# Optimization experiments

Measured on AMD Instinct MI355X. Metric: run time of the kernel, lower is better.

Reference implementation:

```python
import jax, jax.numpy as jnp
import numpy as np

R = 16
ALPHA = 32
SCALING = ALPHA / R  # 2.0


def setup_inputs() -> dict:
    key = jax.random.key(0)
    k_x, k_w, k_b, k_a, k_bm = jax.random.split(key, 5)
    d = 1024
    x = jax.random.normal(k_x, (4, 4096, d), dtype=jnp.float32)
    W = jax.random.normal(k_w, (d, d), dtype=jnp.float32) * 0.02
    b = jax.random.normal(k_b, (d,), dtype=jnp.float32) * 0.02
    A = jax.random.normal(k_a, (R, d), dtype=jnp.float32) * 0.02
    B = jax.random.normal(k_bm, (d, R), dtype=jnp.float32) * 0.02
    return {"x": x, "W": W, "b": b, "A": A, "B": B}


def reference(x, W, b, A, B):
    # base linear: x @ W^T + b   (W: [out, in])
    base = jnp.einsum("bsd,od->bso", x, W) + b
    # low-rank update: (x @ A^T) @ B^T, scaled (dropout p=0 -> identity)
    u = jnp.einsum("bsd,rd->bsr", x, A)   # [B, S, r]
    update = jnp.einsum("bsr,or->bso", u, B)
    return base + SCALING * update
```

## Files before the change

kernel.cpp:

```cpp
#include <hip/hip_runtime.h>


typedef __bf16 bf16x8 __attribute__((ext_vector_type(8)));
typedef float f32x4 __attribute__((ext_vector_type(4)));
typedef unsigned short ushort8 __attribute__((ext_vector_type(8)));

__device__ __forceinline__ unsigned short f2bf(float f) {
    __bf16 h = (__bf16)f;
    union { __bf16 b; unsigned short u; } v; v.b = h; return v.u;
}
__device__ __forceinline__ ushort8 cvt8(f32x4 a, f32x4 b) {
    ushort8 o;
#pragma unroll
    for (int i = 0; i < 4; ++i) { o[i] = f2bf(a[i]); o[i + 4] = f2bf(b[i]); }
    return o;
}
__device__ __forceinline__ void gld16(const unsigned short* g, unsigned short* l) {
    __builtin_amdgcn_global_load_lds(
        (const __attribute__((address_space(1))) unsigned int*)g,
        (__attribute__((address_space(3))) unsigned int*)l, 16, 0, 0);
}

__global__ __launch_bounds__(256) void prep(
    const float* __restrict__ X, const float* __restrict__ W,
    const float* __restrict__ A, const float* __restrict__ B,
    unsigned short* __restrict__ xbf, unsigned short* __restrict__ Weff)
{
    const int b = blockIdx.x;
    if (b < 512) {
        const int idx = b * 256 + threadIdx.x;
        const int o  = idx >> 7;
        const int kc = (idx & 127) << 3;
        float br[16];
#pragma unroll
        for (int r = 0; r < 16; ++r) br[r] = 2.0f * B[o * 16 + r];
        float acc[8];
        const float* wrow = W + (size_t)o * 1024 + kc;
#pragma unroll
        for (int j = 0; j < 8; ++j) acc[j] = wrow[j];
#pragma unroll
        for (int r = 0; r < 16; ++r) {
            const float* arow = A + r * 1024 + kc;
#pragma unroll
            for (int j = 0; j < 8; ++j) acc[j] += br[r] * arow[j];
        }
        ushort8 o8;
#pragma unroll
        for (int j = 0; j < 8; ++j) o8[j] = f2bf(acc[j]);
        *(ushort8*)(Weff + (size_t)o * 1024 + kc) = o8;
    } else {
        const size_t i = ((size_t)(b - 512) * 256 + threadIdx.x) * 8;
        f32x4 a = *(const f32x4*)(X + i);
        f32x4 c = *(const f32x4*)(X + i + 4);
        *(ushort8*)(xbf + i) = cvt8(a, c);
    }
}

template <bool XF32>
__global__ __launch_bounds__(256) void gemm_bt(
    const void* __restrict__ X_,
    const unsigned short* __restrict__ Wt,
    const float* __restrict__ bias,
    float* __restrict__ out)
{
    __shared__ __align__(16) unsigned short lA[128 * 32];
    __shared__ __align__(16) unsigned short lB[128 * 32];

    const int t    = threadIdx.x;
    const int lane = t & 63;
    const int w    = t >> 6;
    const int bm   = blockIdx.x * 128;
    const int bn   = blockIdx.y * 128;
    const int wm   = (w & 1) * 64;
    const int wn   = (w >> 1) * 64;
    const int r16  = lane & 15;
    const int quad = lane >> 4;

    const int srow = t >> 2;
    const int gc   = (t & 3) ^ ((srow >> 1) & 3);
    unsigned short* lsA = lA + t * 8;
    unsigned short* lsB = lB + t * 8;
    const size_t ga0 = (size_t)(bm + srow) * 1024 + gc * 8;
    const size_t ga1 = (size_t)(bm + srow + 64) * 1024 + gc * 8;
    const unsigned short* gB0 = Wt + (size_t)(bn + srow) * 1024 + gc * 8;

    const int p    = (quad ^ ((r16 >> 1) & 3)) * 8;
    const int aoff = (wm + r16) * 32 + p;
    const int boff = (wn + r16) * 32 + p;

    const unsigned short* Xb = (const unsigned short*)X_;
    const float*          Xf = (const float*)X_;

    f32x4 acc[4][4];
#pragma unroll
    for (int i = 0; i < 4; ++i)
#pragma unroll
        for (int j = 0; j < 4; ++j) {
            f32x4 z = {0.f, 0.f, 0.f, 0.f};
            acc[i][j] = z;
        }

    for (int kt = 0; kt < 1024; kt += 32) {
        if (XF32) {
            f32x4 a0 = *(const f32x4*)(Xf + ga0 + kt);
            f32x4 a1 = *(const f32x4*)(Xf + ga0 + kt + 4);
            f32x4 a2 = *(const f32x4*)(Xf + ga1 + kt);
            f32x4 a3 = *(const f32x4*)(Xf + ga1 + kt + 4);
            *(ushort8*)lsA          = cvt8(a0, a1);
            *(ushort8*)(lsA + 2048) = cvt8(a2, a3);
        } else {
            gld16(Xb + ga0 + kt, lsA);
            gld16(Xb + ga1 + kt, lsA + 2048);
        }
        gld16(gB0 + kt,             lsB);
        gld16(gB0 + kt + 64 * 1024, lsB + 2048);
        __syncthreads();

        bf16x8 fa[4], fb[4];
#pragma unroll
        for (int mt = 0; mt < 4; ++mt) fa[mt] = *(const bf16x8*)(lA + aoff + mt * 16 * 32);
#pragma unroll
        for (int nt = 0; nt < 4; ++nt) fb[nt] = *(const bf16x8*)(lB + boff + nt * 16 * 32);

#pragma unroll
        for (int mt = 0; mt < 4; ++mt)
#pragma unroll
            for (int nt = 0; nt < 4; ++nt)
                acc[mt][nt] = __builtin_amdgcn_mfma_f32_16x16x32_bf16(
                    fa[mt], fb[nt], acc[mt][nt], 0, 0, 0);

        __syncthreads();
    }

    const int orow0 = bm + wm + quad * 4;
    const int ocol0 = bn + wn + r16;
#pragma unroll
    for (int nt = 0; nt < 4; ++nt) {
        const float bv = bias[ocol0 + nt * 16];
#pragma unroll
        for (int mt = 0; mt < 4; ++mt)
#pragma unroll
            for (int i = 0; i < 4; ++i)
                out[(size_t)(orow0 + mt * 16 + i) * 1024 + (ocol0 + nt * 16)] =
                    acc[mt][nt][i] + bv;
    }
}

extern "C" void kernel_launch(void* const* d_in, const int* in_sizes, int n_in,
                              void* d_out, int out_size, void* d_ws, size_t ws_size,
                              hipStream_t stream) {
    const float* x  = (const float*)d_in[0];
    const float* W  = (const float*)d_in[1];
    const float* b  = (const float*)d_in[2];
    const float* A  = (const float*)d_in[3];
    const float* Bm = (const float*)d_in[4];
    float* out = (float*)d_out;

    const int M = in_sizes[0] / 1024;
    dim3 grid(M / 128, 1024 / 128);

    const bool fast = ws_size >= ((size_t)(M)*1024*2 + (2u << 20) + 4096);
    if (fast) {
        unsigned short* xbf  = (unsigned short*)d_ws;
        unsigned short* Weff = xbf + (size_t)M * 1024;
        hipLaunchKernelGGL(prep, dim3(512 + M / 2), dim3(256), 0, stream,
                           x, W, A, Bm, xbf, Weff);
        hipLaunchKernelGGL((gemm_bt<false>), grid, dim3(256), 0, stream,
                           (const void*)xbf, Weff, b, out);
    } else {
        unsigned short* Weff = (unsigned short*)d_ws;
        hipLaunchKernelGGL(prep, dim3(512), dim3(256), 0, stream,
                           x, W, A, Bm, (unsigned short*)nullptr, Weff);
        hipLaunchKernelGGL((gemm_bt<true>), grid, dim3(256), 0, stream,
                           (const void*)x, Weff, b, out);
    }
}
```

Before: 166.6 us.

## Replace 128x128 GEMM with 256x256 double-buffered 8-wave pipelined kernel

Adds a new bf16 GEMM kernel with 256x256 output tiles, 512 threads and a 64-wide K step. It double-buffers 128KB of LDS and issues global-to-LDS prefetches two K steps ahead, interleaved with four MFMA phases that are bracketed by barriers and setprio. Block indices are swizzled for L2 locality, and the fast path now requires M to be a multiple of 256. The goal is more data reuse per tile and overlap of memory traffic with MFMA work. In exchange it uses heavy LDS, relies on manual vmcnt accounting, and leaves only 256 blocks, which may underfill the CUs.

```diff
diff --git a/kernel.cpp b/kernel.cpp
--- a/kernel.cpp
+++ b/kernel.cpp
@@ -20,6 +20,9 @@
         (const __attribute__((address_space(1))) unsigned int*)g,
         (__attribute__((address_space(3))) unsigned int*)l, 16, 0, 0);
 }
+
+#define FENCE() asm volatile("" ::: "memory")
+#define BARRIER() do { FENCE(); __builtin_amdgcn_s_barrier(); FENCE(); } while (0)
 
 __global__ __launch_bounds__(256) void prep(
     const float* __restrict__ X, const float* __restrict__ W,
@@ -56,12 +59,159 @@
     }
 }
 
-template <bool XF32>
-__global__ __launch_bounds__(256) void gemm_bt(
-    const void* __restrict__ X_,
+template<int MH, int NH>
+__device__ __forceinline__ void qmfma(f32x4 (&acc)[8][4],
+                                      const bf16x8 (&fa)[8][2],
+                                      const bf16x8 (&fb)[4][2]) {
+#pragma unroll
+    for (int m2 = 0; m2 < 4; ++m2)
+#pragma unroll
+        for (int n2 = 0; n2 < 2; ++n2)
+#pragma unroll
+            for (int ks = 0; ks < 2; ++ks)
+                acc[MH * 4 + m2][NH * 2 + n2] = __builtin_amdgcn_mfma_f32_16x16x32_bf16(
+                    fa[MH * 4 + m2][ks], fb[NH * 2 + n2][ks],
+                    acc[MH * 4 + m2][NH * 2 + n2], 0, 0, 0);
+}
+
+#define PHASE_MFMA(MH, NH)                                          \
+    do { BARRIER();                                                 \
+         asm volatile("s_waitcnt lgkmcnt(0)" ::: "memory");         \
+         __builtin_amdgcn_sched_barrier(0);            \
+         __builtin_amdgcn_s_setprio(1);                             \
+         qmfma<MH, NH>(acc, fa, fb);                                \
+         __builtin_amdgcn_s_setprio(0);                             \
+         BARRIER(); } while (0)
+
+__global__ __launch_bounds__(512, 2) void gemm256(
+    const unsigned short* __restrict__ Xb,
     const unsigned short* __restrict__ Wt,
     const float* __restrict__ bias,
     float* __restrict__ out)
+{
+    extern __shared__ __align__(16) unsigned short lds[];
+
+    const int t    = threadIdx.x;
+    const int lane = t & 63;
+    const int w    = t >> 6;
+    const int wr   = w >> 2;
+    const int wc   = w & 3;
+    const int r16  = lane & 15;
+    const int quad = lane >> 4;
+
+    const int nwg = gridDim.x;
+    int swz = blockIdx.x;
+    if ((nwg & 7) == 0) swz = (swz & 7) * (nwg >> 3) + (swz >> 3);
+    const int bm = (swz >> 2) * 256;
+    const int bn = (swz & 3) * 256;
+
+    const int c0 = w * 128 + lane, c1 = c0 + 64;
+    const int r0 = c0 >> 3,        r1 = c1 >> 3;
+    const int s0c = (c0 & 7) ^ (r0 & 7);
+    const int s1c = (c1 & 7) ^ (r1 & 7);
+    const unsigned short* pA0 = Xb + (size_t)(bm + r0) * 1024 + s0c * 8;
+    const unsigned short* pA1 = Xb + (size_t)(bm + r1) * 1024 + s1c * 8;
+    const unsigned short* pB0 = Wt + (size_t)(bn + r0) * 1024 + s0c * 8;
+    const unsigned short* pB1 = Wt + (size_t)(bn + r1) * 1024 + s1c * 8;
+    const int lc0 = c0 * 8, lc1 = c1 * 8;
+
+    const int ck    = (quad ^ (r16 & 7)) * 8;
+    const int aBase = wr * 8192 + r16 * 64 + ck;
+    const int bBase = 16384 + (wc >> 1) * 8192 + (wc & 1) * 4096 + r16 * 64 + ck;
+
+    f32x4 acc[8][4];
+#pragma unroll
+    for (int i = 0; i < 8; ++i)
+#pragma unroll
+        for (int jj = 0; jj < 4; ++jj)
+            acc[i][jj] = (f32x4){0.f, 0.f, 0.f, 0.f};
+
+    gld16(pA0,               lds + lc0);            gld16(pA1,               lds + lc1);            FENCE();
+    gld16(pA0 + 131072,      lds + 8192  + lc0);    gld16(pA1 + 131072,      lds + 8192  + lc1);    FENCE();
+    gld16(pB0,               lds + 16384 + lc0);    gld16(pB1,               lds + 16384 + lc1);    FENCE();
+    gld16(pB0 + 131072,      lds + 24576 + lc0);    gld16(pB1 + 131072,      lds + 24576 + lc1);    FENCE();
+    gld16(pA0 + 64,          lds + 32768 + lc0);    gld16(pA1 + 64,          lds + 32768 + lc1);    FENCE();
+    gld16(pA0 + 131072 + 64, lds + 40960 + lc0);    gld16(pA1 + 131072 + 64, lds + 40960 + lc1);    FENCE();
+    gld16(pB0 + 64,          lds + 49152 + lc0);    gld16(pB1 + 64,          lds + 49152 + lc1);
+    asm volatile("s_waitcnt vmcnt(6)" ::: "memory");
+    BARRIER();
+
+#pragma unroll 2
+    for (int j = 0; j < 16; ++j) {
+        const unsigned short* Lb = lds + (j & 1) * 32768;
+        unsigned short* Sc = lds + (j & 1) * 32768;
+        unsigned short* Sn = lds + ((j & 1) ^ 1) * 32768;
+        const int k1 = (j + 1) * 64, k2 = (j + 2) * 64;
+
+        bf16x8 fa[8][2], fb[4][2];
+
+#pragma unroll
+        for (int mt = 0; mt < 4; ++mt) {
+            fa[mt][0] = *(const bf16x8*)(Lb + aBase + mt * 1024);
+            fa[mt][1] = *(const bf16x8*)(Lb + (aBase ^ 32) + mt * 1024);
+        }
+#pragma unroll
+        for (int nt = 0; nt < 2; ++nt) {
+            fb[nt][0] = *(const bf16x8*)(Lb + bBase + nt * 1024);
+            fb[nt][1] = *(const bf16x8*)(Lb + (bBase ^ 32) + nt * 1024);
+        }
+        if (wr == 0) {
+#pragma unroll
+            for (int mt = 4; mt < 8; ++mt) {
+                fa[mt][0] = *(const bf16x8*)(Lb + aBase + mt * 1024);
+                fa[mt][1] = *(const bf16x8*)(Lb + (aBase ^ 32) + mt * 1024);
+            }
+        }
+        if (j < 15) { gld16(pB0 + 131072 + k1, Sn + 24576 + lc0);
+                      gld16(pB1 + 131072 + k1, Sn + 24576 + lc1); }
+        PHASE_MFMA(0, 0);
+
+        if (wr == 1) {
+#pragma unroll
+            for (int mt = 4; mt < 8; ++mt) {
+                fa[mt][0] = *(const bf16x8*)(Lb + aBase + mt * 1024);
+                fa[mt][1] = *(const bf16x8*)(Lb + (aBase ^ 32) + mt * 1024);
+            }
+        }
+#pragma unroll
+        for (int nt = 2; nt < 4; ++nt) {
+            fb[nt][0] = *(const bf16x8*)(Lb + bBase + nt * 1024);
+            fb[nt][1] = *(const bf16x8*)(Lb + (bBase ^ 32) + nt * 1024);
+        }
+        if (j < 14) { gld16(pA0 + k2, Sc + lc0);
+                      gld16(pA1 + k2, Sc + lc1); }
+        PHASE_MFMA(0, 1);
+
+        if (j < 14) { gld16(pA0 + 131072 + k2, Sc + 8192 + lc0);
+                      gld16(pA1 + 131072 + k2, Sc + 8192 + lc1); }
+        PHASE_MFMA(1, 1);
+
+        if (j < 14) { gld16(pB0 + k2, Sc + 16384 + lc0);
+                      gld16(pB1 + k2, Sc + 16384 + lc1); }
+        if (j < 14)       asm volatile("s_waitcnt vmcnt(6)" ::: "memory");
+        else if (j == 14) asm volatile("s_waitcnt vmcnt(0)" ::: "memory");
+        PHASE_MFMA(1, 0);
+    }
+
+    const int orow0 = bm + wr * 128 + quad * 4;
+    const int ocol0 = bn + wc * 64 + r16;
+#pragma unroll
+    for (int nt = 0; nt < 4; ++nt) {
+        const float bv = bias[ocol0 + nt * 16];
+#pragma unroll
+        for (int mt = 0; mt < 8; ++mt) {
+            float* orow = out + (size_t)(orow0 + mt * 16) * 1024 + (ocol0 + nt * 16);
+#pragma unroll
+            for (int i = 0; i < 4; ++i)
+                orow[(size_t)i * 1024] = acc[mt][nt][i] + bv;
+        }
+    }
+}
+
+template <bool XF32>
+__global__ __launch_bounds__(256) void gemm_bt(
+    const void* __restrict__ X_, const unsigned short* __restrict__ Wt,
+    const float* __restrict__ bias, float* __restrict__ out)
 {
     __shared__ __align__(16) unsigned short lA[128 * 32];
     __shared__ __align__(16) unsigned short lB[128 * 32];
@@ -157,21 +307,21 @@
     float* out = (float*)d_out;
 
     const int M = in_sizes[0] / 1024;
-    dim3 grid(M / 128, 1024 / 128);
-
-    const bool fast = ws_size >= ((size_t)(M)*1024*2 + (2u << 20) + 4096);
+
+    const bool fast = (ws_size >= ((size_t)(M)*1024*2 + (2u << 20) + 4096)) &&
+                      (M % 256 == 0);
     if (fast) {
         unsigned short* xbf  = (unsigned short*)d_ws;
         unsigned short* Weff = xbf + (size_t)M * 1024;
         hipLaunchKernelGGL(prep, dim3(512 + M / 2), dim3(256), 0, stream,
                            x, W, A, Bm, xbf, Weff);
-        hipLaunchKernelGGL((gemm_bt<false>), grid, dim3(256), 0, stream,
-                           (const void*)xbf, Weff, b, out);
+        hipLaunchKernelGGL(gemm256, dim3((M / 256) * 4), dim3(512), 131072, stream,
+                           xbf, Weff, b, out);
     } else {
         unsigned short* Weff = (unsigned short*)d_ws;
         hipLaunchKernelGGL(prep, dim3(512), dim3(256), 0, stream,
                            x, W, A, Bm, (unsigned short*)nullptr, Weff);
-        hipLaunchKernelGGL((gemm_bt<true>), grid, dim3(256), 0, stream,
+        hipLaunchKernelGGL((gemm_bt<true>), dim3(M / 128, 8), dim3(256), 0, stream,
                            (const void*)x, Weff, b, out);
     }
 }
```

Result: slower. 174.9 us (+5.0%).

## Add double-buffered 256x128 GEMM kernel with split-phase MFMA scheduling

Applied to the files above, without the earlier changes.

Replaces the bf16 GEMM on the fast path with a new 512-thread kernel using 256x128 tiles, double-buffered LDS filled by global_load_lds prefetch two k-steps ahead, and explicit barriers with waitcnt so loads overlap MFMA phases. It also raises MFMA priority with s_setprio and remaps block indices in groups of eight for cache locality. The aim is to hide global load latency that the old single-buffered kernel exposed at each k-step. The fast path now also requires M divisible by 256, and the hand-placed waitcnt and barrier ordering is fragile.

```diff
diff --git a/kernel.cpp b/kernel.cpp
--- a/kernel.cpp
+++ b/kernel.cpp
@@ -20,6 +20,9 @@
         (const __attribute__((address_space(1))) unsigned int*)g,
         (__attribute__((address_space(3))) unsigned int*)l, 16, 0, 0);
 }
+
+#define FENCE() asm volatile("" ::: "memory")
+#define BARRIER() do { FENCE(); __builtin_amdgcn_s_barrier(); FENCE(); } while (0)
 
 __global__ __launch_bounds__(256) void prep(
     const float* __restrict__ X, const float* __restrict__ W,
@@ -56,12 +59,115 @@
     }
 }
 
-template <bool XF32>
-__global__ __launch_bounds__(256) void gemm_bt(
-    const void* __restrict__ X_,
+#define PHASE_MFMA(LO)                                              \
+    do { BARRIER();                                                 \
+         asm volatile("s_waitcnt lgkmcnt(0)" ::: "memory");         \
+         __builtin_amdgcn_sched_barrier(0);            \
+         __builtin_amdgcn_s_setprio(1);                             \
+         _Pragma("unroll")                                          \
+         for (int m2 = 0; m2 < 4; ++m2)                             \
+             _Pragma("unroll")                                      \
+             for (int n2 = 0; n2 < 2; ++n2)                         \
+                 acc[(LO) + m2][n2] = __builtin_amdgcn_mfma_f32_16x16x32_bf16( \
+                     fa[(LO) + m2], fb[n2], acc[(LO) + m2][n2], 0, 0, 0);      \
+         __builtin_amdgcn_s_setprio(0);                             \
+         BARRIER(); } while (0)
+
+__global__ __launch_bounds__(512, 4) void gemm256(
+    const unsigned short* __restrict__ Xb,
     const unsigned short* __restrict__ Wt,
     const float* __restrict__ bias,
     float* __restrict__ out)
+{
+    extern __shared__ __align__(16) unsigned short lds[];
+
+    const int t    = threadIdx.x;
+    const int lane = t & 63;
+    const int w    = t >> 6;
+    const int wr   = w >> 2;
+    const int wc   = w & 3;
+    const int r16  = lane & 15;
+    const int quad = lane >> 4;
+
+    const int nwg = gridDim.x;
+    int swz = blockIdx.x;
+    if ((nwg & 7) == 0) swz = (swz & 7) * (nwg >> 3) + (swz >> 3);
+    const int bm = (swz >> 3) * 256;
+    const int bn = (swz & 7) * 128;
+
+    const int r  = t >> 2;
+    const int sc = (t & 3) ^ (r & 3);
+    const unsigned short* pA0 = Xb + (size_t)(bm + r) * 1024 + sc * 8;
+    const unsigned short* pA1 = pA0 + 131072;
+    const unsigned short* pB  = Wt + (size_t)(bn + r) * 1024 + sc * 8;
+    const int lc = t * 8;
+
+    const int sw = (quad ^ (r16 & 3)) * 8;
+    const int aB = wr * 512 + r16 * 32 + sw;
+    const int bB = wc * 512 + r16 * 32 + sw;
+
+    f32x4 acc[8][2];
+#pragma unroll
+    for (int i = 0; i < 8; ++i)
+#pragma unroll
+        for (int jj = 0; jj < 2; ++jj)
+            acc[i][jj] = (f32x4){0.f, 0.f, 0.f, 0.f};
+
+    gld16(pA0,      lds + lc);                 FENCE();
+    gld16(pB,       lds + 8192 + lc);          FENCE();
+    gld16(pA1,      lds + 4096 + lc);          FENCE();
+    gld16(pA0 + 32, lds + 12288 + lc);         FENCE();
+    gld16(pB  + 32, lds + 12288 + 8192 + lc);
+    asm volatile("s_waitcnt vmcnt(2)" ::: "memory");
+    BARRIER();
+
+#pragma unroll 2
+    for (int j = 0; j < 32; ++j) {
+        const int cur  = (j & 1) * 12288;
+        const int next = cur ^ 12288;
+        const unsigned short* Lb = lds + cur;
+        const int k1 = (j + 1) * 32, k2 = (j + 2) * 32;
+
+        bf16x8 fa[8], fb[2];
+
+#pragma unroll
+        for (int mt = 0; mt < 4; ++mt)
+            fa[mt] = *(const bf16x8*)(Lb + mt * 1024 + aB);
+#pragma unroll
+        for (int nt = 0; nt < 2; ++nt)
+            fb[nt] = *(const bf16x8*)(Lb + 8192 + nt * 2048 + bB);
+        if (j < 31) gld16(pA1 + k1, lds + next + 4096 + lc);
+        PHASE_MFMA(0);
+
+#pragma unroll
+        for (int mt = 4; mt < 8; ++mt)
+            fa[mt] = *(const bf16x8*)(Lb + 4096 + (mt - 4) * 1024 + aB);
+        if (j < 30) { gld16(pA0 + k2, lds + cur + lc);              FENCE();
+                      gld16(pB  + k2, lds + cur + 8192 + lc); }
+        if (j < 30)       asm volatile("s_waitcnt vmcnt(2)" ::: "memory");
+        else if (j == 30) asm volatile("s_waitcnt vmcnt(0)" ::: "memory");
+        PHASE_MFMA(4);
+    }
+
+    const int orow0 = bm + wr * 16 + quad * 4;
+    const int ocol0 = bn + wc * 16 + r16;
+#pragma unroll
+    for (int nt = 0; nt < 2; ++nt) {
+        const float bv = bias[ocol0 + nt * 64];
+#pragma unroll
+        for (int mt = 0; mt < 8; ++mt) {
+            float* orow = out + (size_t)(orow0 + mt * 32) * 1024 + (ocol0 + nt * 64);
+#pragma unroll
+            for (int i = 0; i < 4; ++i)
+                orow[(size_t)i * 1024] = acc[mt][nt][i] + bv;
+        }
+    }
+}
+
+template <bool XF32>
+__global__ __launch_bounds__(256) void gemm_bt(
+    const void* __restrict__ X_, const unsigned short* __restrict__ Wt,
+    const float* __restrict__ bias, float* __restrict__ out)
 {
     __shared__ __align__(16) unsigned short lA[128 * 32];
     __shared__ __align__(16) unsigned short lB[128 * 32];
@@ -157,21 +263,21 @@
     float* out = (float*)d_out;
 
     const int M = in_sizes[0] / 1024;
-    dim3 grid(M / 128, 1024 / 128);
-
-    const bool fast = ws_size >= ((size_t)(M)*1024*2 + (2u << 20) + 4096);
+
+    const bool fast = (ws_size >= ((size_t)(M)*1024*2 + (2u << 20) + 4096)) &&
+                      (M % 256 == 0);
     if (fast) {
         unsigned short* xbf  = (unsigned short*)d_ws;
         unsigned short* Weff = xbf + (size_t)M * 1024;
         hipLaunchKernelGGL(prep, dim3(512 + M / 2), dim3(256), 0, stream,
                            x, W, A, Bm, xbf, Weff);
-        hipLaunchKernelGGL((gemm_bt<false>), grid, dim3(256), 0, stream,
-                           (const void*)xbf, Weff, b, out);
+        hipLaunchKernelGGL(gemm256, dim3((M / 256) * 8), dim3(512), 49152, stream,
+                           xbf, Weff, b, out);
     } else {
         unsigned short* Weff = (unsigned short*)d_ws;
         hipLaunchKernelGGL(prep, dim3(512), dim3(256), 0, stream,
                            x, W, A, Bm, (unsigned short*)nullptr, Weff);
-        hipLaunchKernelGGL((gemm_bt<true>), grid, dim3(256), 0, stream,
+        hipLaunchKernelGGL((gemm_bt<true>), dim3(M / 128, 8), dim3(256), 0, stream,
                            (const void*)x, Weff, b, out);
     }
 }
```

New measurement: 155.6 us. 1.07x faster.

## Add triple-buffered 512-thread GEMM with async LDS loads and tile swizzle

Applied to the files above, without the earlier changes.

Replaces the single-buffered 256-thread bf16 GEMM with a 512-thread kernel that uses three LDS stages filled by global_load_lds, so the next tiles load while MFMAs run. It uses explicit vmcnt waits, raw s_barrier and setprio, and remaps block indices so blocks sharing a weight column tile run close together for L2 reuse. Each wave now computes a 32x64 output tile, which cuts register pressure to allow more resident waves. The cost is 48KB of dynamic LDS and hand-tuned wait counts that could be fragile.

```diff
diff --git a/kernel.cpp b/kernel.cpp
--- a/kernel.cpp
+++ b/kernel.cpp
@@ -9,17 +9,20 @@
     __bf16 h = (__bf16)f;
     union { __bf16 b; unsigned short u; } v; v.b = h; return v.u;
 }
-__device__ __forceinline__ ushort8 cvt8(f32x4 a, f32x4 b) {
+__device__ __forceinline__ ushort8 cvt8u(f32x4 a, f32x4 b) {
     ushort8 o;
 #pragma unroll
     for (int i = 0; i < 4; ++i) { o[i] = f2bf(a[i]); o[i + 4] = f2bf(b[i]); }
     return o;
 }
-__device__ __forceinline__ void gld16(const unsigned short* g, unsigned short* l) {
+__device__ __forceinline__ void gld16(const void* g, void* l) {
     __builtin_amdgcn_global_load_lds(
         (const __attribute__((address_space(1))) unsigned int*)g,
         (__attribute__((address_space(3))) unsigned int*)l, 16, 0, 0);
 }
+
+#define FENCE() asm volatile("" ::: "memory")
+#define BARRIER() do { FENCE(); __builtin_amdgcn_s_barrier(); FENCE(); } while (0)
 
 __global__ __launch_bounds__(256) void prep(
     const float* __restrict__ X, const float* __restrict__ W,
@@ -52,16 +55,113 @@
         const size_t i = ((size_t)(b - 512) * 256 + threadIdx.x) * 8;
         f32x4 a = *(const f32x4*)(X + i);
         f32x4 c = *(const f32x4*)(X + i + 4);
-        *(ushort8*)(xbf + i) = cvt8(a, c);
-    }
-}
-
-template <bool XF32>
-__global__ __launch_bounds__(256) void gemm_bt(
-    const void* __restrict__ X_,
+        *(ushort8*)(xbf + i) = cvt8u(a, c);
+    }
+}
+
+__global__ __launch_bounds__(512, 6) void gemm256(
+    const unsigned short* __restrict__ Xb,
     const unsigned short* __restrict__ Wt,
     const float* __restrict__ bias,
     float* __restrict__ out)
+{
+    extern __shared__ __align__(16) char lds[];
+
+    const int t    = threadIdx.x;
+    const int lane = t & 63;
+    const int w    = t >> 6;
+    const int wr   = w & 3;
+    const int wc   = w >> 2;
+    const int r16  = lane & 15;
+    const int quad = lane >> 4;
+
+    const int nwg = gridDim.x;
+    int swz = blockIdx.x;
+    if ((nwg & 7) == 0) swz = (swz & 7) * (nwg >> 3) + (swz >> 3);
+    const int bm = (swz >> 3) * 128;
+    const int bn = (swz & 7) * 128;
+
+    const int ar = t >> 2;
+    const int ac = (t & 3) ^ ((ar >> 1) & 3);
+    const unsigned short* gA = Xb + (size_t)(bm + ar) * 1024 + ac * 8;
+    const unsigned short* gB = Wt + (size_t)(bn + ar) * 1024 + ac * 8;
+    const int adst = t * 16;
+
+    const int sw = (quad ^ ((r16 >> 1) & 3)) * 16;
+    const int aB = wr * 1024 + r16 * 64 + sw;
+    const int bB = 8192 + wc * 1024 + r16 * 64 + sw;
+
+    f32x4 acc[2][4];
+#pragma unroll
+    for (int i = 0; i < 2; ++i)
+#pragma unroll
+        for (int jj = 0; jj < 4; ++jj)
+            acc[i][jj] = (f32x4){0.f, 0.f, 0.f, 0.f};
+
+#define STAGE(BUF, K)                                                           \
+    do { gld16(gA + (K), lds + (BUF) + adst);        FENCE();                   \
+         gld16(gB + (K), lds + (BUF) + 8192 + adst); FENCE(); } while (0)
+
+#define TILE(J, RB, SB, STG, VM)                                                \
+    do {                                                                        \
+        const char* Lb = lds + (RB);                                            \
+        bf16x8 fa[2], fb[4];                                                    \
+        fa[0] = *(const bf16x8*)(Lb + aB);                                      \
+        fa[1] = *(const bf16x8*)(Lb + aB + 4096);                               \
+        _Pragma("unroll")                                                       \
+        for (int nt = 0; nt < 4; ++nt)                                          \
+            fb[nt] = *(const bf16x8*)(Lb + bB + nt * 2048);                     \
+        if (STG) STAGE((SB), ((J) + 2) * 32);                                   \
+        if ((VM) == 2)      asm volatile("s_waitcnt vmcnt(2)" ::: "memory");    \
+        else if ((VM) == 0) asm volatile("s_waitcnt vmcnt(0)" ::: "memory");    \
+        asm volatile("s_waitcnt lgkmcnt(0)" ::: "memory");                      \
+        BARRIER();                                                              \
+        __builtin_amdgcn_sched_barrier(0);                         \
+        __builtin_amdgcn_s_setprio(1);                                          \
+        _Pragma("unroll")                                                       \
+        for (int mt = 0; mt < 2; ++mt)                                          \
+            _Pragma("unroll")                                                   \
+            for (int nt = 0; nt < 4; ++nt)                                      \
+                acc[mt][nt] = __builtin_amdgcn_mfma_f32_16x16x32_bf16(          \
+                    fa[mt], fb[nt], acc[mt][nt], 0, 0, 0);                      \
+        __builtin_amdgcn_s_setprio(0);                                          \
+    } while (0)
+
+    STAGE(0, 0);
+    STAGE(16384, 32);
+    asm volatile("s_waitcnt vmcnt(2)" ::: "memory");
+    BARRIER();
+
+    for (int jj = 0; jj < 30; jj += 3) {
+        TILE(jj + 0, 0,     32768, 1, 2);
+        TILE(jj + 1, 16384, 0,     1, 2);
+        TILE(jj + 2, 32768, 16384, 1, 2);
+    }
+    TILE(30, 0,     0, 0, 0);
+    TILE(31, 16384, 0, 0, -1);
+
+#undef TILE
+#undef STAGE
+
+    const int orow0 = bm + wr * 16 + quad * 4;
+    const int ocol0 = bn + wc * 16 + r16;
+#pragma unroll
+    for (int nt = 0; nt < 4; ++nt) {
+        const float bv = bias[ocol0 + nt * 32];
+#pragma unroll
+        for (int mt = 0; mt < 2; ++mt) {
+            float* orow = out + (size_t)(orow0 + mt * 64) * 1024 + (ocol0 + nt * 32);
+#pragma unroll
+            for (int i = 0; i < 4; ++i)
+                orow[(size_t)i * 1024] = acc[mt][nt][i] + bv;
+        }
+    }
+}
+
+template <bool XF32>
+__global__ __launch_bounds__(256) void gemm_bt(
+    const void* __restrict__ X_, const unsigned short* __restrict__ Wt,
+    const float* __restrict__ bias, float* __restrict__ out)
 {
     __shared__ __align__(16) unsigned short lA[128 * 32];
     __shared__ __align__(16) unsigned short lB[128 * 32];
@@ -106,8 +206,8 @@
             f32x4 a1 = *(const f32x4*)(Xf + ga0 + kt + 4);
             f32x4 a2 = *(const f32x4*)(Xf + ga1 + kt);
             f32x4 a3 = *(const f32x4*)(Xf + ga1 + kt + 4);
-            *(ushort8*)lsA          = cvt8(a0, a1);
-            *(ushort8*)(lsA + 2048) = cvt8(a2, a3);
+            *(ushort8*)lsA          = cvt8u(a0, a1);
+            *(ushort8*)(lsA + 2048) = cvt8u(a2, a3);
         } else {
             gld16(Xb + ga0 + kt, lsA);
             gld16(Xb + ga1 + kt, lsA + 2048);
@@ -157,21 +257,21 @@
     float* out = (float*)d_out;
 
     const int M = in_sizes[0] / 1024;
-    dim3 grid(M / 128, 1024 / 128);
-
-    const bool fast = ws_size >= ((size_t)(M)*1024*2 + (2u << 20) + 4096);
+
+    const bool fast = (ws_size >= ((size_t)(M)*1024*2 + (2u << 20) + 4096)) &&
+                      (M % 128 == 0);
     if (fast) {
         unsigned short* xbf  = (unsigned short*)d_ws;
         unsigned short* Weff = xbf + (size_t)M * 1024;
         hipLaunchKernelGGL(prep, dim3(512 + M / 2), dim3(256), 0, stream,
                            x, W, A, Bm, xbf, Weff);
-        hipLaunchKernelGGL((gemm_bt<false>), grid, dim3(256), 0, stream,
-                           (const void*)xbf, Weff, b, out);
+        hipLaunchKernelGGL(gemm256, dim3((M / 128) * 8), dim3(512), 49152, stream,
+                           xbf, Weff, b, out);
     } else {
         unsigned short* Weff = (unsigned short*)d_ws;
         hipLaunchKernelGGL(prep, dim3(512), dim3(256), 0, stream,
                            x, W, A, Bm, (unsigned short*)nullptr, Weff);
-        hipLaunchKernelGGL((gemm_bt<true>), grid, dim3(256), 0, stream,
+        hipLaunchKernelGGL((gemm_bt<true>), dim3(M / 128, 8), dim3(256), 0, stream,
                            (const void*)x, Weff, b, out);
     }
 }
```

After: 159.2 us. 4.5% less time.
